# Kernel optimization log

Hardware: AMD Instinct MI355X
Metric: run time of the kernel (lower is better)

## Reference

```python
import jax, jax.numpy as jnp
import numpy as np

D_MODEL, D_STATE, N_HEADS = 1024, 64, 16


def setup_inputs() -> dict:
    key = jax.random.key(0)
    ks = jax.random.split(key, 4)
    B, T = 4, 4096
    s = 1.0 / np.sqrt(D_MODEL)
    x = jax.random.normal(ks[0], (B, T, D_MODEL), dtype=jnp.float32)
    h_prev = jnp.zeros((B, N_HEADS, D_STATE), dtype=jnp.float32)
    gate_w = jax.random.normal(ks[1], (2 * N_HEADS * D_STATE, D_MODEL), dtype=jnp.float32) * s
    # torch init: forget-gate bias = 1, input-gate bias = 0
    gate_b = jnp.concatenate([jnp.ones(N_HEADS * D_STATE), jnp.zeros(N_HEADS * D_STATE)]).astype(jnp.float32)
    value_w = jax.random.normal(ks[2], (N_HEADS * D_STATE, D_MODEL), dtype=jnp.float32) * s
    out_w = jax.random.normal(ks[3], (D_MODEL, N_HEADS * D_STATE), dtype=jnp.float32) * s
    return {"x": x, "h_prev": h_prev, "gate_w": gate_w, "gate_b": gate_b, "value_w": value_w, "out_w": out_w}


def reference(x, h_prev, gate_w, gate_b, value_w, out_w):
    B, T, _ = x.shape
    H, S = N_HEADS, D_STATE
    gates = (jnp.einsum('btd,gd->btg', x, gate_w) + gate_b).reshape(B, T, 2, H, S)
    A = jax.nn.sigmoid(gates[:, :, 0])   # [B,T,H,S] forget gate
    Bg = jax.nn.sigmoid(gates[:, :, 1])  # [B,T,H,S] input gate
    V = jnp.einsum('btd,vd->btv', x, value_w).reshape(B, T, H, S)

    def step(h, inp):
        a_t, bv_t = inp
        h = a_t * h + bv_t
        return h, h

    # time-major for scan; precompute B*V elementwise product
    a_tm = jnp.moveaxis(A, 1, 0)                # [T,B,H,S]
    bv_tm = jnp.moveaxis(Bg * V, 1, 0)          # [T,B,H,S]
    h_last, h_seq = jax.lax.scan(step, h_prev, (a_tm, bv_tm))
    h_flat = jnp.moveaxis(h_seq, 0, 1).reshape(B, T, H * S)
    y = jnp.einsum('btv,dv->btd', h_flat, out_w)  # dropout is identity at p=0/eval
    return y, h_last
```

## Files before the change

### kernel.cpp

```cpp
#include <hip/hip_runtime.h>
#include <cstdint>
#include <cstddef>


typedef _Float16 f16;
typedef _Float16 f16x2 __attribute__((ext_vector_type(2)));
typedef _Float16 f16x8 __attribute__((ext_vector_type(8)));
typedef float    f32x4 __attribute__((ext_vector_type(4)));

__device__ __forceinline__ void gload_lds16(const void* g, void* l) {
  __builtin_amdgcn_global_load_lds(
      (const __attribute__((address_space(1))) void*)g,
      (__attribute__((address_space(3))) void*)l, 16, 0, 0);
}

__device__ __forceinline__ float sigmoidf_(float x) {
  return 1.0f / (1.0f + __expf(-x));
}

__global__ __launch_bounds__(256) void cast_pack(
    const float* __restrict__ x, const float* __restrict__ gw,
    const float* __restrict__ vw, const float* __restrict__ ow,
    f16* __restrict__ xh, f16* __restrict__ wgv, f16* __restrict__ owb) {
  const int XG = 2097152, GG = 262144, VG = 131072, OG = 131072;
  int id = blockIdx.x * 256 + threadIdx.x;
  const float* src;
  f16* dst;
  if (id < XG) {
    src = x + (size_t)id * 8;
    dst = xh + (size_t)id * 8;
  } else if (id < XG + GG) {
    int g = id - XG;
    int row = g >> 7, col = g & 127;
    int drow = (row < 1024) ? row : (1024 + 2 * (row - 1024));
    src = gw + ((size_t)row << 10) + col * 8;
    dst = wgv + ((size_t)drow << 10) + col * 8;
  } else if (id < XG + GG + VG) {
    int g = id - XG - GG;
    int row = g >> 7, col = g & 127;
    int drow = 1024 + 2 * row + 1;
    src = vw + ((size_t)row << 10) + col * 8;
    dst = wgv + ((size_t)drow << 10) + col * 8;
  } else if (id < XG + GG + VG + OG) {
    int g = id - XG - GG - VG;
    src = ow + (size_t)g * 8;
    dst = owb + (size_t)g * 8;
  } else {
    return;
  }
  float4 v0 = ((const float4*)src)[0], v1 = ((const float4*)src)[1];
  f16x8 o;
  o[0] = (f16)v0.x; o[1] = (f16)v0.y; o[2] = (f16)v0.z; o[3] = (f16)v0.w;
  o[4] = (f16)v1.x; o[5] = (f16)v1.y; o[6] = (f16)v1.z; o[7] = (f16)v1.w;
  *(f16x8*)dst = o;
}

#define DSREAD(dst, addr, off)                                        \
  asm volatile("ds_read_b128 %0, %1 offset:%2"                       \
               : "=v"(dst)                                            \
               : "v"(addr), "i"(off))

#define WAIT_LGKM(n)                                                  \
  asm volatile("s_waitcnt lgkmcnt(" #n ")" ::: "memory");             \
  __builtin_amdgcn_sched_barrier(0)

#define SBAR asm volatile("s_barrier" ::: "memory")

template <int EPI>
__global__ __launch_bounds__(512, 2) void gemm256(
    const f16* __restrict__ A, const f16* __restrict__ Bw,
    const float* __restrict__ gate_b, void* __restrict__ o0v,
    void* __restrict__ o1v, int Mtiles) {
  constexpr int K = 1024;
  __shared__ __align__(16) f16 SH[65536];
  f16* LA = SH;
  f16* LB = SH + 32768;

  const int tid  = threadIdx.x;
  const int lane = tid & 63;
  const int l15  = lane & 15;
  const int oct4 = lane >> 4;
  const int wid  = tid >> 6;
  const int wr   = wid >> 2;
  const int wc   = wid & 3;

  const int nwg = gridDim.x;
  const int bid = blockIdx.x;
  const int swz = (bid & 7) * (nwg >> 3) + (bid >> 3);
  const int m0 = (swz % Mtiles) * 256;
  const int n0 = (swz / Mtiles) * 256;

  const int srow = tid >> 2;
  const int soct = (tid & 3) ^ ((srow >> 1) & 3);
  const f16* Ag = A  + (size_t)(n0 + srow) * K + soct * 8;
  const f16* Bg = Bw + (size_t)(m0 + srow) * K + soct * 8;
  f16* Al = LA + tid * 8;
  f16* Bl = LB + tid * 8;

  const int fswz  = oct4 ^ ((l15 >> 1) & 3);
  const unsigned shbase = (unsigned)(uintptr_t)(&SH[0]);
  const int aaddr = (int)shbase + ((wr * 128 + l15) * 4 + fswz) * 16;
  const int baddr = (int)shbase + 65536 + ((wc * 64 + l15) * 4 + fswz) * 16;

  f32x4 acc[8][4];
#pragma unroll
  for (int mm = 0; mm < 8; ++mm)
#pragma unroll
    for (int nn = 0; nn < 4; ++nn)
#pragma unroll
      for (int e = 0; e < 4; ++e) acc[mm][nn][e] = 0.f;

#define STAGE_AB(kt)                                                  \
  do {                                                                \
    const f16* sa_ = Ag + (kt) * 32;                                  \
    const f16* sb_ = Bg + (kt) * 32;                                  \
    f16* da_ = Al + ((kt) & 3) * 8192;                                \
    f16* db_ = Bl + ((kt) & 3) * 8192;                                \
    gload_lds16(sa_, da_);                                            \
    gload_lds16(sa_ + 128 * K, da_ + 4096);                           \
    gload_lds16(sb_, db_);                                            \
    gload_lds16(sb_ + 128 * K, db_ + 4096);                           \
  } while (0)

  STAGE_AB(0);
  STAGE_AB(1);
  STAGE_AB(2);
  asm volatile("s_waitcnt vmcnt(8)" ::: "memory");
  SBAR;
  __builtin_amdgcn_sched_barrier(0);

  f16x8 af[8], bf[4];
  DSREAD(bf[0], baddr, 0);    DSREAD(bf[1], baddr, 1024);
  DSREAD(bf[2], baddr, 2048); DSREAD(bf[3], baddr, 3072);
  DSREAD(af[0], aaddr, 0);    DSREAD(af[1], aaddr, 1024);
  DSREAD(af[2], aaddr, 2048); DSREAD(af[3], aaddr, 3072);
  DSREAD(af[4], aaddr, 4096); DSREAD(af[5], aaddr, 5120);
  DSREAD(af[6], aaddr, 6144); DSREAD(af[7], aaddr, 7168);

#pragma unroll
  for (int kt = 0; kt < 32; ++kt) {
    if (kt <= 28) STAGE_AB(kt + 3);

    __builtin_amdgcn_s_setprio(1);
    WAIT_LGKM(7);
#pragma unroll
    for (int nn = 0; nn < 4; ++nn)
      acc[0][nn] = __builtin_amdgcn_mfma_f32_16x16x32_f16(
          af[0], bf[nn], acc[0][nn], 0, 0, 0);
    WAIT_LGKM(4);
#pragma unroll
    for (int mm = 1; mm < 4; ++mm)
#pragma unroll
      for (int nn = 0; nn < 4; ++nn)
        acc[mm][nn] = __builtin_amdgcn_mfma_f32_16x16x32_f16(
            af[mm], bf[nn], acc[mm][nn], 0, 0, 0);
    WAIT_LGKM(0);
#pragma unroll
    for (int mm = 4; mm < 8; ++mm)
#pragma unroll
      for (int nn = 0; nn < 4; ++nn)
        acc[mm][nn] = __builtin_amdgcn_mfma_f32_16x16x32_f16(
            af[mm], bf[nn], acc[mm][nn], 0, 0, 0);
    __builtin_amdgcn_s_setprio(0);
    __builtin_amdgcn_sched_barrier(0);

    if (kt < 31) {
      if (kt <= 28) {
        asm volatile("s_waitcnt vmcnt(8)" ::: "memory");
      } else if (kt == 29) {
        asm volatile("s_waitcnt vmcnt(4)" ::: "memory");
      } else {
        asm volatile("s_waitcnt vmcnt(0)" ::: "memory");
      }
      SBAR;
      __builtin_amdgcn_sched_barrier(0);
      const int ro = ((kt + 1) & 3) * 16384;
      const int aP = aaddr + ro;
      const int bP = baddr + ro;
      DSREAD(bf[0], bP, 0);    DSREAD(bf[1], bP, 1024);
      DSREAD(bf[2], bP, 2048); DSREAD(bf[3], bP, 3072);
      DSREAD(af[0], aP, 0);    DSREAD(af[1], aP, 1024);
      DSREAD(af[2], aP, 2048); DSREAD(af[3], aP, 3072);
      DSREAD(af[4], aP, 4096); DSREAD(af[5], aP, 5120);
      DSREAD(af[6], aP, 6144); DSREAD(af[7], aP, 7168);
    }
  }
#undef STAGE_AB

  if (EPI == 1) {
    float* out = (float*)o0v;
#pragma unroll
    for (int mm = 0; mm < 8; ++mm)
#pragma unroll
      for (int nn = 0; nn < 4; ++nn) {
        const int m = m0 + wc * 64 + nn * 16 + l15;
#pragma unroll
        for (int r = 0; r < 4; ++r) {
          const int n = n0 + wr * 128 + mm * 16 + oct4 * 4 + r;
          out[(size_t)n * 1024 + m] = acc[mm][nn][r];
        }
      }
    return;
  }

  if (m0 < 1024) {
    float bias[4];
#pragma unroll
    for (int nn = 0; nn < 4; ++nn)
      bias[nn] = gate_b[m0 + wc * 64 + nn * 16 + l15];
    f16* o0 = (f16*)o0v;
#pragma unroll
    for (int ck = 0; ck < 2; ++ck) {
      __builtin_amdgcn_s_barrier();
      asm volatile("" ::: "memory");
      if (wr == ck) {
#pragma unroll
        for (int mm = 0; mm < 8; ++mm)
#pragma unroll
          for (int nn = 0; nn < 4; ++nn) {
            const int ch = wc * 64 + nn * 16 + l15;
#pragma unroll
            for (int r = 0; r < 4; ++r) {
              const int nl = mm * 16 + oct4 * 4 + r;
              SH[nl * 264 + ch] = (f16)sigmoidf_(acc[mm][nn][r] + bias[nn]);
            }
          }
      }
      __builtin_amdgcn_s_barrier();
      asm volatile("" ::: "memory");
#pragma unroll
      for (int j = 0; j < 8; ++j) {
        int s = j * 512 + tid;
        int row = s >> 5, sl = s & 31;
        f16x8 vv = *(const f16x8*)&SH[row * 264 + sl * 8];
        *(f16x8*)(o0 + (size_t)(n0 + ck * 128 + row) * 1024 + m0 + sl * 8) =
            vv;
      }
    }
  } else {
    const int c0 = (m0 - 1024) >> 1;
    float biasv[4];
#pragma unroll
    for (int nn = 0; nn < 4; ++nn) {
      const int ml = wc * 64 + nn * 16 + l15;
      biasv[nn] = gate_b[1024 + c0 + (ml >> 1)];
    }
    f16* o1 = (f16*)o1v;
#pragma unroll
    for (int ck = 0; ck < 2; ++ck) {
      __builtin_amdgcn_s_barrier();
      asm volatile("" ::: "memory");
      if (wr == ck) {
#pragma unroll
        for (int mm = 0; mm < 8; ++mm)
#pragma unroll
          for (int nn = 0; nn < 4; ++nn) {
            const int ml = wc * 64 + nn * 16 + l15;
#pragma unroll
            for (int r = 0; r < 4; ++r) {
              float val = acc[mm][nn][r];
              float pv = __shfl_xor(val, 1, 64);
              if (!(lane & 1)) {
                const int nl = mm * 16 + oct4 * 4 + r;
                SH[nl * 136 + (ml >> 1)] =
                    (f16)(sigmoidf_(val + biasv[nn]) * pv);
              }
            }
          }
      }
      __builtin_amdgcn_s_barrier();
      asm volatile("" ::: "memory");
#pragma unroll
      for (int j = 0; j < 4; ++j) {
        int s = j * 512 + tid;
        int row = s >> 4, sl = s & 15;
        f16x8 vv = *(const f16x8*)&SH[row * 136 + sl * 8];
        *(f16x8*)(o1 + (size_t)(n0 + ck * 128 + row) * 1024 + c0 + sl * 8) =
            vv;
      }
    }
  }
}

__global__ __launch_bounds__(256) void scan_pass1(
    const f16x2* __restrict__ a, const f16x2* __restrict__ bv,
    float2* __restrict__ Ac, float2* __restrict__ Uc) {
  const int c2 = blockIdx.x * 256 + threadIdx.x;
  const int j = blockIdx.y;
  const int b = blockIdx.z;
  const size_t base = ((size_t)(b * 4096 + j * 32)) * 512 + c2;
  float P0 = 1.f, P1 = 1.f, U0 = 0.f, U1 = 0.f;
#pragma unroll 8
  for (int t = 0; t < 32; ++t) {
    const size_t o = base + (size_t)t * 512;
    f16x2 at = a[o], bt = bv[o];
    float a0 = (float)at[0], a1 = (float)at[1];
    P0 *= a0; P1 *= a1;
    U0 = a0 * U0 + (float)bt[0];
    U1 = a1 * U1 + (float)bt[1];
  }
  const size_t o = ((size_t)(b * 128 + j)) * 512 + c2;
  Ac[o] = make_float2(P0, P1);
  Uc[o] = make_float2(U0, U1);
}

__global__ __launch_bounds__(256) void scan_pass2(
    const float* __restrict__ Ac, const float* __restrict__ Uc,
    const float* __restrict__ h_prev, float* __restrict__ Hs,
    float* __restrict__ hlast) {
  __shared__ float SA[4][64], SU[4][64];
  const int tid = threadIdx.x;
  const int seg = tid >> 6;
  const int cl  = tid & 63;
  const int ch  = blockIdx.x * 64 + cl;
  const int b = ch >> 10, c = ch & 1023;
  float A = 1.f, U = 0.f;
  for (int t = 0; t < 32; ++t) {
    const int j = seg * 32 + t;
    const size_t o = ((size_t)(b * 128 + j)) * 1024 + c;
    float av = Ac[o], uv = Uc[o];
    U = av * U + uv;
    A = av * A;
  }
  SA[seg][cl] = A;
  SU[seg][cl] = U;
  __syncthreads();
  float Ae = 1.f, Ue = 0.f;
  for (int s = 0; s < seg; ++s) {
    float av = SA[s][cl], uv = SU[s][cl];
    Ue = av * Ue + uv;
    Ae = av * Ae;
  }
  float H = Ae * h_prev[b * 1024 + c] + Ue;
  for (int t = 0; t < 32; ++t) {
    const int j = seg * 32 + t;
    const size_t o = ((size_t)(b * 128 + j)) * 1024 + c;
    Hs[o] = H;
    H = Ac[o] * H + Uc[o];
  }
  if (seg == 3) hlast[b * 1024 + c] = H;
}

__global__ __launch_bounds__(256) void scan_pass3(
    const f16x2* __restrict__ a, const f16x2* __restrict__ bv,
    const float2* __restrict__ Hs, f16x2* __restrict__ hb) {
  const int c2 = blockIdx.x * 256 + threadIdx.x;
  const int j = blockIdx.y;
  const int b = blockIdx.z;
  const size_t base = ((size_t)(b * 4096 + j * 32)) * 512 + c2;
  float2 H = Hs[((size_t)(b * 128 + j)) * 512 + c2];
  float h0 = H.x, h1 = H.y;
#pragma unroll 8
  for (int t = 0; t < 32; ++t) {
    const size_t o = base + (size_t)t * 512;
    f16x2 at = a[o], bt = bv[o];
    h0 = (float)at[0] * h0 + (float)bt[0];
    h1 = (float)at[1] * h1 + (float)bt[1];
    f16x2 hv; hv[0] = (f16)h0; hv[1] = (f16)h1;
    hb[o] = hv;
  }
}

extern "C" void kernel_launch(void* const* d_in, const int* in_sizes, int n_in,
                              void* d_out, int out_size, void* d_ws,
                              size_t ws_size, hipStream_t stream) {
  const float* x       = (const float*)d_in[0];
  const float* h_prev  = (const float*)d_in[1];
  const float* gate_w  = (const float*)d_in[2];
  const float* gate_b  = (const float*)d_in[3];
  const float* value_w = (const float*)d_in[4];
  const float* out_w   = (const float*)d_in[5];
  float* out = (float*)d_out;

  char* ws = (char*)d_ws;
  f16*   xh   = (f16*)(ws);
  f16*   wgv  = (f16*)(ws + 33554432);
  f16*   owb  = (f16*)(ws + 39845888);
  f16*   abuf = (f16*)(ws + 41943040);
  f16*   bvb  = (f16*)(ws + 75497472);
  float* Ac   = (float*)(ws + 109051904);
  float* Uc   = (float*)(ws + 111149056);
  float* Hs   = (float*)(ws + 113246208);
  float* hlast = out + 16777216;

  cast_pack<<<10240, 256, 0, stream>>>(x, gate_w, value_w, out_w, xh, wgv,
                                       owb);

  gemm256<0><<<dim3(768), 512, 0, stream>>>(xh, wgv, gate_b, abuf, bvb, 12);

  scan_pass1<<<dim3(2, 128, 4), 256, 0, stream>>>(
      (const f16x2*)abuf, (const f16x2*)bvb, (float2*)Ac, (float2*)Uc);
  scan_pass2<<<64, 256, 0, stream>>>(Ac, Uc, h_prev, Hs, hlast);
  scan_pass3<<<dim3(2, 128, 4), 256, 0, stream>>>(
      (const f16x2*)abuf, (const f16x2*)bvb, (const float2*)Hs, (f16x2*)xh);

  gemm256<1><<<dim3(256), 512, 0, stream>>>(xh, owb, nullptr, out, nullptr, 4);
}
```

Measured before the change: 372.0 us.

## Replace direct global-to-LDS loads with register-staged global loads and ds_write

The GEMM mainloop stops using global_load_lds (buffer-to-LDS DMA) with a 3-stage-ahead prefetch. Instead it loads each tile into VGPRs with global_load_dwordx4 one stage ahead, then writes it to LDS with ds_write_b128 after the MFMA block. This gives explicit control over write timing, but it shortens prefetch depth to one stage and adds VGPR pressure plus extra LDS write instructions. A full vmcnt(0) wait now sits in every iteration.

```diff
diff --git a/kernel.cpp b/kernel.cpp
--- a/kernel.cpp
+++ b/kernel.cpp
@@ -7,12 +7,6 @@
 typedef _Float16 f16x2 __attribute__((ext_vector_type(2)));
 typedef _Float16 f16x8 __attribute__((ext_vector_type(8)));
 typedef float    f32x4 __attribute__((ext_vector_type(4)));
-
-__device__ __forceinline__ void gload_lds16(const void* g, void* l) {
-  __builtin_amdgcn_global_load_lds(
-      (const __attribute__((address_space(1))) void*)g,
-      (__attribute__((address_space(3))) void*)l, 16, 0, 0);
-}
 
 __device__ __forceinline__ float sigmoidf_(float x) {
   return 1.0f / (1.0f + __expf(-x));
@@ -60,8 +54,21 @@
                : "=v"(dst)                                            \
                : "v"(addr), "i"(off))
 
+#define DSW(addr, src, off)                                           \
+  asm volatile("ds_write_b128 %0, %1 offset:%2"                      \
+               :: "v"(addr), "v"(src), "i"(off))
+
+#define GLOAD(dst, ptr)                                               \
+  asm volatile("global_load_dwordx4 %0, %1, off"                     \
+               : "=v"(dst)                                            \
+               : "v"(ptr))
+
 #define WAIT_LGKM(n)                                                  \
   asm volatile("s_waitcnt lgkmcnt(" #n ")" ::: "memory");             \
+  __builtin_amdgcn_sched_barrier(0)
+
+#define WAIT_VM0                                                      \
+  asm volatile("s_waitcnt vmcnt(0)" ::: "memory");                    \
   __builtin_amdgcn_sched_barrier(0)
 
 #define SBAR asm volatile("s_barrier" ::: "memory")
@@ -73,8 +80,6 @@
     void* __restrict__ o1v, int Mtiles) {
   constexpr int K = 1024;
   __shared__ __align__(16) f16 SH[65536];
-  f16* LA = SH;
-  f16* LB = SH + 32768;
 
   const int tid  = threadIdx.x;
   const int lane = tid & 63;
@@ -92,13 +97,16 @@
 
   const int srow = tid >> 2;
   const int soct = (tid & 3) ^ ((srow >> 1) & 3);
-  const f16* Ag = A  + (size_t)(n0 + srow) * K + soct * 8;
-  const f16* Bg = Bw + (size_t)(m0 + srow) * K + soct * 8;
-  f16* Al = LA + tid * 8;
-  f16* Bl = LB + tid * 8;
+  const f16* AgL = A  + (size_t)(n0 + srow) * K + soct * 8;
+  const f16* AgH = AgL + (size_t)128 * K;
+  const f16* BgL = Bw + (size_t)(m0 + srow) * K + soct * 8;
+  const f16* BgH = BgL + (size_t)128 * K;
+
+  const unsigned shbase = (unsigned)(uintptr_t)(&SH[0]);
+  const int awr = (int)shbase + tid * 16;
+  const int bwr = (int)shbase + 65536 + tid * 16;
 
   const int fswz  = oct4 ^ ((l15 >> 1) & 3);
-  const unsigned shbase = (unsigned)(uintptr_t)(&SH[0]);
   const int aaddr = (int)shbase + ((wr * 128 + l15) * 4 + fswz) * 16;
   const int baddr = (int)shbase + 65536 + ((wc * 64 + l15) * 4 + fswz) * 16;
 
@@ -110,22 +118,30 @@
 #pragma unroll
       for (int e = 0; e < 4; ++e) acc[mm][nn][e] = 0.f;
 
-#define STAGE_AB(kt)                                                  \
+  f16x8 ga0, ga1, gb0, gb1;
+
+#define STAGE_LOAD(kt)                                                \
   do {                                                                \
-    const f16* sa_ = Ag + (kt) * 32;                                  \
-    const f16* sb_ = Bg + (kt) * 32;                                  \
-    f16* da_ = Al + ((kt) & 3) * 8192;                                \
-    f16* db_ = Bl + ((kt) & 3) * 8192;                                \
-    gload_lds16(sa_, da_);                                            \
-    gload_lds16(sa_ + 128 * K, da_ + 4096);                           \
-    gload_lds16(sb_, db_);                                            \
-    gload_lds16(sb_ + 128 * K, db_ + 4096);                           \
+    const f16* pa_ = AgL + (kt) * 32;                                 \
+    const f16* pA2 = AgH + (kt) * 32;                                 \
+    const f16* pb_ = BgL + (kt) * 32;                                 \
+    const f16* pB2 = BgH + (kt) * 32;                                 \
+    GLOAD(ga0, pa_); GLOAD(ga1, pA2);                                 \
+    GLOAD(gb0, pb_); GLOAD(gb1, pB2);                                 \
   } while (0)
 
-  STAGE_AB(0);
-  STAGE_AB(1);
-  STAGE_AB(2);
-  asm volatile("s_waitcnt vmcnt(8)" ::: "memory");
+#define STAGE_WRITE(kt)                                               \
+  do {                                                                \
+    const int wo_ = ((kt) & 3) * 16384;                               \
+    DSW(awr + wo_, ga0, 0); DSW(awr + wo_, ga1, 8192);                \
+    DSW(bwr + wo_, gb0, 0); DSW(bwr + wo_, gb1, 8192);                \
+  } while (0)
+
+  STAGE_LOAD(0);
+  WAIT_VM0;
+  STAGE_WRITE(0);
+  WAIT_LGKM(0);
+  STAGE_LOAD(1);
   SBAR;
   __builtin_amdgcn_sched_barrier(0);
 
@@ -139,8 +155,6 @@
 
 #pragma unroll
   for (int kt = 0; kt < 32; ++kt) {
-    if (kt <= 28) STAGE_AB(kt + 3);
-
     __builtin_amdgcn_s_setprio(1);
     WAIT_LGKM(7);
 #pragma unroll
@@ -164,14 +178,11 @@
     __builtin_amdgcn_s_setprio(0);
     __builtin_amdgcn_sched_barrier(0);
 
-    if (kt < 31) {
-      if (kt <= 28) {
-        asm volatile("s_waitcnt vmcnt(8)" ::: "memory");
-      } else if (kt == 29) {
-        asm volatile("s_waitcnt vmcnt(4)" ::: "memory");
-      } else {
-        asm volatile("s_waitcnt vmcnt(0)" ::: "memory");
-      }
+    if (kt <= 30) {
+      WAIT_VM0;
+      STAGE_WRITE(kt + 1);
+      WAIT_LGKM(0);
+      if (kt <= 29) STAGE_LOAD(kt + 2);
       SBAR;
       __builtin_amdgcn_sched_barrier(0);
       const int ro = ((kt + 1) & 3) * 16384;
@@ -185,7 +196,8 @@
       DSREAD(af[6], aP, 6144); DSREAD(af[7], aP, 7168);
     }
   }
-#undef STAGE_AB
+#undef STAGE_LOAD
+#undef STAGE_WRITE
 
   if (EPI == 1) {
     float* out = (float*)o0v;
```

Measured after the change: 366.0 us. Within noise of the previous version (-1.6%).
